# Performance work log

Measured on AMD Instinct MI355X. Metric: run time of the kernel, lower is better.

## Reference

```python
import jax, jax.numpy as jnp
import numpy as np

N_NODES = 50000
N_EDGES = 800000
D_IN, D_HID, D_OUT = 128, 256, 128


def _glorot(key, shape):
    fan_in, fan_out = shape[1], shape[0]
    lim = (6.0 / (fan_in + fan_out)) ** 0.5
    return jax.random.uniform(key, shape, jnp.float32, -lim, lim)


def setup_inputs() -> dict:
    key = jax.random.key(0)
    ks = jax.random.split(key, 8)
    x = jax.random.normal(ks[0], (N_NODES, D_IN), dtype=jnp.float32)
    edge_index = jax.random.randint(ks[1], (2, N_EDGES), 0, N_NODES, dtype=jnp.int64)
    # Layer 1: SAGEConv(D_IN -> D_HID); Layer 2: SAGEConv(D_HID -> D_OUT)
    # PyG SAGEConv: out = lin_l(mean_aggr(x_j)) + lin_r(x); bias lives in lin_l.
    Wl1 = _glorot(ks[2], (D_HID, D_IN))
    bl1 = jnp.zeros((D_HID,), jnp.float32)
    Wr1 = _glorot(ks[3], (D_HID, D_IN))
    Wl2 = _glorot(ks[4], (D_OUT, D_HID))
    bl2 = jnp.zeros((D_OUT,), jnp.float32)
    Wr2 = _glorot(ks[5], (D_OUT, D_HID))
    return {"x": x, "Wl1": Wl1, "bl1": bl1, "Wr1": Wr1,
            "Wl2": Wl2, "bl2": bl2, "Wr2": Wr2, "edge_index": edge_index}


def _sage_conv(x, src, dst, deg_inv, Wl, bl, Wr):
    # gather source features per edge, sum into dst buckets, normalize by in-degree
    msg_sum = jax.ops.segment_sum(x[src], dst, num_segments=N_NODES)  # [N, d_in]
    mean = msg_sum * deg_inv  # mean aggregation; isolated nodes -> zeros
    return mean @ Wl.T + bl + x @ Wr.T


def reference(x, Wl1, bl1, Wr1, Wl2, bl2, Wr2, edge_index):
    src, dst = edge_index[0], edge_index[1]
    deg = jax.ops.segment_sum(jnp.ones((N_EDGES,), jnp.float32), dst,
                              num_segments=N_NODES)
    deg_inv = (1.0 / jnp.maximum(deg, 1.0))[:, None]  # [N, 1]
    h = _sage_conv(x, src, dst, deg_inv, Wl1, bl1, Wr1)
    h = jax.nn.relu(h)  # dropout is identity in eval mode
    out = _sage_conv(h, src, dst, deg_inv, Wl2, bl2, Wr2)
    return out
```

## Files before the change

### kernel.cpp

```cpp
#include <hip/hip_runtime.h>
#include <hip/hip_fp16.h>

#define N_NODES 50000
#define N_EDGES 800000
#define D_IN 128
#define D_HID 256
#define D_OUT 128
#define NCHUNK 196
#define GEMM_GRID 512

typedef _Float16 f16x8 __attribute__((ext_vector_type(8)));
typedef float f32x4 __attribute__((ext_vector_type(4)));


__device__ __forceinline__ void cvt8(const float* __restrict__ src,
                                     __half* __restrict__ dstp, int i) {
    const float4* s4 = (const float4*)src;
    float4 a = s4[i * 2];
    float4 b = s4[i * 2 + 1];
    float4 o;
    __half2* op = (__half2*)&o;
    op[0] = __float22half2_rn(make_float2(a.x, a.y));
    op[1] = __float22half2_rn(make_float2(a.z, a.w));
    op[2] = __float22half2_rn(make_float2(b.x, b.y));
    op[3] = __float22half2_rn(make_float2(b.z, b.w));
    ((float4*)dstp)[i] = o;
}

__global__ __launch_bounds__(256)
void prep_kernel(const float* __restrict__ x, __half* __restrict__ xb,
                 const float* __restrict__ Wl1, const float* __restrict__ Wr1,
                 const float* __restrict__ Wl2, const float* __restrict__ Wr2,
                 __half* __restrict__ wl1h, __half* __restrict__ wr1h,
                 __half* __restrict__ wl2h, __half* __restrict__ wr2h,
                 int* __restrict__ deg) {
    int b = blockIdx.x;
    if (b < 3125) {
        int i = b * 256 + threadIdx.x;
        cvt8(x, xb, i);
    } else if (b < 3141) {
        int i = (b - 3125) * 256 + threadIdx.x;
        cvt8(Wl1, wl1h, i);
        cvt8(Wr1, wr1h, i);
        cvt8(Wl2, wl2h, i);
        cvt8(Wr2, wr2h, i);
    } else {
        int i = (b - 3141) * 256 + threadIdx.x;
        if (i < N_NODES) deg[i] = 0;
    }
}


__global__ void deg_rank_kernel(const int* __restrict__ dst, int* __restrict__ deg,
                                int* __restrict__ rank) {
    int i = blockIdx.x * blockDim.x + threadIdx.x;
    if (i < N_EDGES) rank[i] = atomicAdd(&deg[dst[i]], 1);
}

__global__ void chunk_sum(const int* __restrict__ deg, int* __restrict__ partial) {
    __shared__ int s[256];
    int i = blockIdx.x * 256 + threadIdx.x;
    s[threadIdx.x] = (i < N_NODES) ? deg[i] : 0;
    __syncthreads();
    for (int off = 128; off > 0; off >>= 1) {
        if (threadIdx.x < off) s[threadIdx.x] += s[threadIdx.x + off];
        __syncthreads();
    }
    if (threadIdx.x == 0) partial[blockIdx.x] = s[0];
}

__global__ void scatter_scan(const int* __restrict__ deg, const int* __restrict__ partial,
                             int* __restrict__ row_ptr, float* __restrict__ deg_inv) {
    __shared__ int s[256];
    __shared__ int base_s;
    const int tid = threadIdx.x;
    const int bid = blockIdx.x;
    s[tid] = (tid < bid) ? partial[tid] : 0;
    __syncthreads();
    for (int off = 128; off > 0; off >>= 1) {
        if (tid < off) s[tid] += s[tid + off];
        __syncthreads();
    }
    if (tid == 0) base_s = s[0];
    __syncthreads();
    int i = bid * 256 + tid;
    int v = (i < N_NODES) ? deg[i] : 0;
    s[tid] = v;
    __syncthreads();
    for (int off = 1; off < 256; off <<= 1) {
        int t = (tid >= off) ? s[tid - off] : 0;
        __syncthreads();
        s[tid] += t;
        __syncthreads();
    }
    if (i < N_NODES) {
        int rp = base_s + s[tid] - v;
        row_ptr[i] = rp;
        deg_inv[i] = 1.0f / fmaxf((float)v, 1.0f);
        if (i == N_NODES - 1) row_ptr[N_NODES] = N_EDGES;
    }
}

__global__ void fill_csr(const int* __restrict__ src, const int* __restrict__ dst,
                         const int* __restrict__ rank, const int* __restrict__ row_ptr,
                         int* __restrict__ csr_src) {
    int e = blockIdx.x * blockDim.x + threadIdx.x;
    if (e < N_EDGES) {
        csr_src[row_ptr[dst[e]] + rank[e]] = src[e];
    }
}


__device__ __forceinline__ void add_row(const float4& v, float2 (&acc)[4]) {
    const __half2* hp = (const __half2*)&v;
    #pragma unroll
    for (int j = 0; j < 4; ++j) {
        float2 f = __half22float2(hp[j]);
        acc[j].x += f.x;
        acc[j].y += f.y;
    }
}

template<bool ACCUM_F32>
__device__ __forceinline__ void gather_core(const __half2* __restrict__ feat,
                                            const int* __restrict__ row_ptr,
                                            const int* __restrict__ csr_src,
                                            const float* __restrict__ deg_inv,
                                            __half2* __restrict__ outh,
                                            float* __restrict__ outf) {
    const float4* feat4 = (const float4*)feat;
    const int lane = threadIdx.x & 63;
    const int g = lane >> 4;
    const int s = lane & 15;
    const int n = blockIdx.x * 4 + (threadIdx.x >> 6);
    const int beg = row_ptr[n];
    const int end = row_ptr[n + 1];
    float2 acc[4] = {};

    int idx = (beg + lane < end) ? csr_src[beg + lane] : 0;
    int base = beg;
    while (base < end) {
        int cnt = end - base;
        if (cnt > 64) cnt = 64;
        const int nbase = base + 64;
        int nidx = (nbase + lane < end) ? csr_src[nbase + lane] : 0;

        int it = 0;
        for (; it + 16 <= cnt; it += 16) {
            int s0 = __shfl(idx, it + g);
            int s1 = __shfl(idx, it + 4 + g);
            int s2 = __shfl(idx, it + 8 + g);
            int s3 = __shfl(idx, it + 12 + g);
            float4 v0 = feat4[(size_t)s0 * 16 + s];
            float4 v1 = feat4[(size_t)s1 * 16 + s];
            float4 v2 = feat4[(size_t)s2 * 16 + s];
            float4 v3 = feat4[(size_t)s3 * 16 + s];
            add_row(v0, acc);
            add_row(v1, acc);
            add_row(v2, acc);
            add_row(v3, acc);
        }
        for (; it + 4 <= cnt; it += 4) {
            int s0 = __shfl(idx, it + g);
            float4 v0 = feat4[(size_t)s0 * 16 + s];
            add_row(v0, acc);
        }
        if (it < cnt) {
            int s0 = __shfl(idx, it + g);
            if (g < cnt - it) {
                float4 v0 = feat4[(size_t)s0 * 16 + s];
                add_row(v0, acc);
            }
        }
        idx = nidx;
        base = nbase;
    }

    #pragma unroll
    for (int j = 0; j < 4; ++j) {
        acc[j].x += __shfl_xor(acc[j].x, 16);
        acc[j].y += __shfl_xor(acc[j].y, 16);
        acc[j].x += __shfl_xor(acc[j].x, 32);
        acc[j].y += __shfl_xor(acc[j].y, 32);
    }
    if (g == 0) {
        float di = deg_inv[n];
        if (ACCUM_F32) {
            float4* orow = (float4*)(outf + (size_t)n * 128);
            float4 o0 = orow[s * 2];
            float4 o1 = orow[s * 2 + 1];
            o0.x += acc[0].x * di; o0.y += acc[0].y * di;
            o0.z += acc[1].x * di; o0.w += acc[1].y * di;
            o1.x += acc[2].x * di; o1.y += acc[2].y * di;
            o1.z += acc[3].x * di; o1.w += acc[3].y * di;
            orow[s * 2] = o0;
            orow[s * 2 + 1] = o1;
        } else {
            float4 o;
            __half2* op = (__half2*)&o;
            op[0] = __float22half2_rn(make_float2(acc[0].x * di, acc[0].y * di));
            op[1] = __float22half2_rn(make_float2(acc[1].x * di, acc[1].y * di));
            op[2] = __float22half2_rn(make_float2(acc[2].x * di, acc[2].y * di));
            op[3] = __float22half2_rn(make_float2(acc[3].x * di, acc[3].y * di));
            ((float4*)(outh + (size_t)n * 64))[s] = o;
        }
    }
}

__global__ __launch_bounds__(256)
void gather_mean_h(const __half2* __restrict__ feat, const int* __restrict__ row_ptr,
                   const int* __restrict__ csr_src, const float* __restrict__ deg_inv,
                   __half2* __restrict__ outv) {
    gather_core<false>(feat, row_ptr, csr_src, deg_inv, outv, nullptr);
}

__global__ __launch_bounds__(256)
void gather_mean_add_f32(const __half2* __restrict__ feat, const int* __restrict__ row_ptr,
                         const int* __restrict__ csr_src, const float* __restrict__ deg_inv,
                         float* __restrict__ out) {
    gather_core<true>(feat, row_ptr, csr_src, deg_inv, nullptr, out);
}


#define HPAD 264

__global__ __launch_bounds__(256, 1)
void gemm_fused(const __half* __restrict__ Aa, const __half* __restrict__ Ba,
                const __half* __restrict__ Ab, const __half* __restrict__ Bb,
                const float* __restrict__ bias1,
                const __half* __restrict__ B20, const __half* __restrict__ B21,
                const float* __restrict__ bias2,
                __half* __restrict__ P, float* __restrict__ out) {
    __shared__ __half hlds[2][16][HPAD];
    const int lane = threadIdx.x & 63;
    const int wave = threadIdx.x >> 6;
    const int quad = lane >> 4;
    const int l16 = lane & 15;
    const int koff = quad * 8;

    f16x8 bf1[2][4][4];
    #pragma unroll
    for (int p = 0; p < 2; ++p) {
        const __half* __restrict__ B = p ? Bb : Ba;
        #pragma unroll
        for (int kc = 0; kc < 4; ++kc)
            #pragma unroll
            for (int nt = 0; nt < 4; ++nt)
                bf1[p][kc][nt] = *(const f16x8*)(
                    B + (size_t)(wave * 64 + nt * 16 + l16) * D_IN + kc * 32 + koff);
    }
    float bv1[4];
    #pragma unroll
    for (int nt = 0; nt < 4; ++nt) bv1[nt] = bias1[wave * 64 + nt * 16 + l16];

    f16x8 bf20[8][2], bf21[8][2];
    #pragma unroll
    for (int kc = 0; kc < 8; ++kc)
        #pragma unroll
        for (int nt = 0; nt < 2; ++nt) {
            size_t brow = (size_t)(wave * 32 + nt * 16 + l16) * D_HID + kc * 32 + koff;
            bf20[kc][nt] = *(const f16x8*)(B20 + brow);
            bf21[kc][nt] = *(const f16x8*)(B21 + brow);
        }
    float bv2[2];
    #pragma unroll
    for (int nt = 0; nt < 2; ++nt) bv2[nt] = bias2[wave * 32 + nt * 16 + l16];

    const int NT = N_NODES / 16;
    const int g = gridDim.x;

    auto loadA = [&](int t, f16x8 (&a)[2][4]) {
        const size_t arow = (size_t)(t * 16 + l16) * D_IN + koff;
        #pragma unroll
        for (int kc = 0; kc < 4; ++kc) {
            a[0][kc] = *(const f16x8*)(Aa + arow + kc * 32);
            a[1][kc] = *(const f16x8*)(Ab + arow + kc * 32);
        }
    };

    auto step = [&](int tile, const f16x8 (&a)[2][4], int buf) {
        f32x4 acc1[4] = {};
        #pragma unroll
        for (int p = 0; p < 2; ++p)
            #pragma unroll
            for (int kc = 0; kc < 4; ++kc)
                #pragma unroll
                for (int nt = 0; nt < 4; ++nt)
                    acc1[nt] = __builtin_amdgcn_mfma_f32_16x16x32_f16(
                        a[p][kc], bf1[p][kc][nt], acc1[nt], 0, 0, 0);
        #pragma unroll
        for (int nt = 0; nt < 4; ++nt) {
            int col = wave * 64 + nt * 16 + l16;
            #pragma unroll
            for (int r = 0; r < 4; ++r)
                hlds[buf][quad * 4 + r][col] =
                    __float2half(fmaxf(acc1[nt][r] + bv1[nt], 0.f));
        }
        __syncthreads();
        f32x4 acc20[2] = {};
        f32x4 acc21[2] = {};
        #pragma unroll
        for (int kc = 0; kc < 8; ++kc) {
            f16x8 a2 = *(const f16x8*)&hlds[buf][l16][kc * 32 + koff];
            #pragma unroll
            for (int nt = 0; nt < 2; ++nt) {
                acc20[nt] = __builtin_amdgcn_mfma_f32_16x16x32_f16(
                    a2, bf20[kc][nt], acc20[nt], 0, 0, 0);
                acc21[nt] = __builtin_amdgcn_mfma_f32_16x16x32_f16(
                    a2, bf21[kc][nt], acc21[nt], 0, 0, 0);
            }
        }
        #pragma unroll
        for (int nt = 0; nt < 2; ++nt) {
            int col = wave * 32 + nt * 16 + l16;
            #pragma unroll
            for (int r = 0; r < 4; ++r) {
                int row = tile * 16 + quad * 4 + r;
                P[(size_t)row * D_OUT + col] = __float2half(acc20[nt][r]);
                out[(size_t)row * D_OUT + col] = acc21[nt][r] + bv2[nt];
            }
        }
    };

    f16x8 A0[2][4], A1[2][4];
    int tile = blockIdx.x;
    int buf = 0;
    loadA(tile, A0);
    while (true) {
        if (tile + g < NT) loadA(tile + g, A1);
        step(tile, A0, buf);
        buf ^= 1;
        tile += g;
        if (tile >= NT) break;
        if (tile + g < NT) loadA(tile + g, A0);
        step(tile, A1, buf);
        buf ^= 1;
        tile += g;
        if (tile >= NT) break;
    }
}

extern "C" void kernel_launch(void* const* d_in, const int* in_sizes, int n_in,
                              void* d_out, int out_size, void* d_ws, size_t ws_size,
                              hipStream_t stream) {
    const float* x   = (const float*)d_in[0];
    const float* Wl1 = (const float*)d_in[1];
    const float* bl1 = (const float*)d_in[2];
    const float* Wr1 = (const float*)d_in[3];
    const float* Wl2 = (const float*)d_in[4];
    const float* bl2 = (const float*)d_in[5];
    const float* Wr2 = (const float*)d_in[6];
    const int*   ei  = (const int*)d_in[7];
    const int* src = ei;
    const int* dst = ei + N_EDGES;
    float* out = (float*)d_out;

    char* w = (char*)d_ws;
    auto alloc = [&](size_t bytes) {
        char* r = w;
        w += (bytes + 255) & ~(size_t)255;
        return r;
    };
    int*     deg       = (int*)alloc((size_t)N_NODES * 4);
    int*     row_ptr   = (int*)alloc((size_t)(N_NODES + 1) * 4);
    int*     rank      = (int*)alloc((size_t)N_EDGES * 4);
    int*     partial   = (int*)alloc(NCHUNK * 4);
    int*     csr_src   = (int*)alloc((size_t)N_EDGES * 4);
    float*   deg_inv   = (float*)alloc((size_t)N_NODES * 4);
    __half2* xb        = (__half2*)alloc((size_t)N_NODES * 64 * 4);
    __half2* mean1     = (__half2*)alloc((size_t)N_NODES * 64 * 4);
    __half2* pb        = (__half2*)alloc((size_t)N_NODES * 64 * 4);
    __half*  wl1h      = (__half*)alloc(4 * 32768 * 2);
    __half*  wr1h = wl1h + 32768;
    __half*  wl2h = wr1h + 32768;
    __half*  wr2h = wl2h + 32768;

    prep_kernel<<<3337, 256, 0, stream>>>(x, (__half*)xb, Wl1, Wr1, Wl2, Wr2,
        wl1h, wr1h, wl2h, wr2h, deg);

    deg_rank_kernel<<<(N_EDGES + 255) / 256, 256, 0, stream>>>(dst, deg, rank);
    chunk_sum<<<NCHUNK, 256, 0, stream>>>(deg, partial);
    scatter_scan<<<NCHUNK, 256, 0, stream>>>(deg, partial, row_ptr, deg_inv);
    fill_csr<<<(N_EDGES + 255) / 256, 256, 0, stream>>>(src, dst, rank, row_ptr, csr_src);

    gather_mean_h<<<12500, 256, 0, stream>>>(xb, row_ptr, csr_src, deg_inv, mean1);

    gemm_fused<<<GEMM_GRID, 256, 0, stream>>>(
        (const __half*)mean1, wl1h, (const __half*)xb, wr1h, bl1,
        wl2h, wr2h, bl2, (__half*)pb, out);

    gather_mean_add_f32<<<12500, 256, 0, stream>>>(pb, row_ptr, csr_src, deg_inv, out);
}
```

Baseline: 239.4 us.

## Fuse degree counting into prep, drop chunk-sum, split GEMM into producer/consumer waves

The degree/rank atomic pass is folded into the conversion kernel, with the degree buffer cleared by a memset. The separate chunk-sum kernel is removed: each scan block now re-sums all preceding degrees itself, which adds redundant global reads that grow with block index. The fused GEMM becomes a 512-thread block where four waves compute layer-1 tiles into double-buffered LDS and four other waves consume them for layer 2, so the two stages overlap. The grid is halved to 256 blocks. This cuts kernel launches and aims to overlap the two GEMM stages, at the cost of extra block barriers and a more serial scan.

```diff
diff --git a/kernel.cpp b/kernel.cpp
--- a/kernel.cpp
+++ b/kernel.cpp
@@ -7,7 +7,8 @@
 #define D_HID 256
 #define D_OUT 128
 #define NCHUNK 196
-#define GEMM_GRID 512
+#define NTILES 3125
+#define GEMM_GRID 256
 
 typedef _Float16 f16x8 __attribute__((ext_vector_type(8)));
 typedef float f32x4 __attribute__((ext_vector_type(4)));
@@ -28,12 +29,13 @@
 }
 
 __global__ __launch_bounds__(256)
-void prep_kernel(const float* __restrict__ x, __half* __restrict__ xb,
-                 const float* __restrict__ Wl1, const float* __restrict__ Wr1,
-                 const float* __restrict__ Wl2, const float* __restrict__ Wr2,
-                 __half* __restrict__ wl1h, __half* __restrict__ wr1h,
-                 __half* __restrict__ wl2h, __half* __restrict__ wr2h,
-                 int* __restrict__ deg) {
+void prep_deg_rank(const float* __restrict__ x, __half* __restrict__ xb,
+                   const float* __restrict__ Wl1, const float* __restrict__ Wr1,
+                   const float* __restrict__ Wl2, const float* __restrict__ Wr2,
+                   __half* __restrict__ wl1h, __half* __restrict__ wr1h,
+                   __half* __restrict__ wl2h, __half* __restrict__ wr2h,
+                   const int* __restrict__ dst, int* __restrict__ deg,
+                   int* __restrict__ rank) {
     int b = blockIdx.x;
     if (b < 3125) {
         int i = b * 256 + threadIdx.x;
@@ -45,37 +47,21 @@
         cvt8(Wl2, wl2h, i);
         cvt8(Wr2, wr2h, i);
     } else {
-        int i = (b - 3141) * 256 + threadIdx.x;
-        if (i < N_NODES) deg[i] = 0;
-    }
-}
-
-
-__global__ void deg_rank_kernel(const int* __restrict__ dst, int* __restrict__ deg,
-                                int* __restrict__ rank) {
-    int i = blockIdx.x * blockDim.x + threadIdx.x;
-    if (i < N_EDGES) rank[i] = atomicAdd(&deg[dst[i]], 1);
-}
-
-__global__ void chunk_sum(const int* __restrict__ deg, int* __restrict__ partial) {
-    __shared__ int s[256];
-    int i = blockIdx.x * 256 + threadIdx.x;
-    s[threadIdx.x] = (i < N_NODES) ? deg[i] : 0;
-    __syncthreads();
-    for (int off = 128; off > 0; off >>= 1) {
-        if (threadIdx.x < off) s[threadIdx.x] += s[threadIdx.x + off];
-        __syncthreads();
-    }
-    if (threadIdx.x == 0) partial[blockIdx.x] = s[0];
-}
-
-__global__ void scatter_scan(const int* __restrict__ deg, const int* __restrict__ partial,
+        int e = (b - 3141) * 256 + threadIdx.x;
+        rank[e] = atomicAdd(&deg[dst[e]], 1);
+    }
+}
+
+
+__global__ void scatter_scan(const int* __restrict__ deg,
                              int* __restrict__ row_ptr, float* __restrict__ deg_inv) {
     __shared__ int s[256];
     __shared__ int base_s;
     const int tid = threadIdx.x;
     const int bid = blockIdx.x;
-    s[tid] = (tid < bid) ? partial[tid] : 0;
+    int sum = 0;
+    for (int j = tid; j < bid * 256; j += 256) sum += deg[j];
+    s[tid] = sum;
     __syncthreads();
     for (int off = 128; off > 0; off >>= 1) {
         if (tid < off) s[tid] += s[tid + off];
@@ -224,119 +210,134 @@
 
 #define HPAD 264
 
-__global__ __launch_bounds__(256, 1)
-void gemm_fused(const __half* __restrict__ Aa, const __half* __restrict__ Ba,
-                const __half* __restrict__ Ab, const __half* __restrict__ Bb,
-                const float* __restrict__ bias1,
-                const __half* __restrict__ B20, const __half* __restrict__ B21,
-                const float* __restrict__ bias2,
-                __half* __restrict__ P, float* __restrict__ out) {
-    __shared__ __half hlds[2][16][HPAD];
+__global__ __launch_bounds__(512, 1)
+void gemm_pc(const __half* __restrict__ Aa,
+             const __half* __restrict__ Ab,
+             const __half* __restrict__ Wl1h, const __half* __restrict__ Wr1h,
+             const float* __restrict__ bias1,
+             const __half* __restrict__ B20, const __half* __restrict__ B21,
+             const float* __restrict__ bias2,
+             __half* __restrict__ P, float* __restrict__ out) {
+    __shared__ __half ldsH[2][16][HPAD];
     const int lane = threadIdx.x & 63;
     const int wave = threadIdx.x >> 6;
     const int quad = lane >> 4;
     const int l16 = lane & 15;
     const int koff = quad * 8;
-
-    f16x8 bf1[2][4][4];
-    #pragma unroll
-    for (int p = 0; p < 2; ++p) {
-        const __half* __restrict__ B = p ? Bb : Ba;
+    const int g = gridDim.x;
+
+    if (wave < 4) {
+        f16x8 bf1[2][4][4];
         #pragma unroll
-        for (int kc = 0; kc < 4; ++kc)
-            #pragma unroll
-            for (int nt = 0; nt < 4; ++nt)
-                bf1[p][kc][nt] = *(const f16x8*)(
-                    B + (size_t)(wave * 64 + nt * 16 + l16) * D_IN + kc * 32 + koff);
-    }
-    float bv1[4];
-    #pragma unroll
-    for (int nt = 0; nt < 4; ++nt) bv1[nt] = bias1[wave * 64 + nt * 16 + l16];
-
-    f16x8 bf20[8][2], bf21[8][2];
-    #pragma unroll
-    for (int kc = 0; kc < 8; ++kc)
+        for (int p = 0; p < 2; ++p) {
+            const __half* __restrict__ B = p ? Wr1h : Wl1h;
+            #pragma unroll
+            for (int kc = 0; kc < 4; ++kc)
+                #pragma unroll
+                for (int nt = 0; nt < 4; ++nt)
+                    bf1[p][kc][nt] = *(const f16x8*)(
+                        B + (size_t)(wave * 64 + nt * 16 + l16) * D_IN + kc * 32 + koff);
+        }
+        float bv1[4];
         #pragma unroll
-        for (int nt = 0; nt < 2; ++nt) {
-            size_t brow = (size_t)(wave * 32 + nt * 16 + l16) * D_HID + kc * 32 + koff;
-            bf20[kc][nt] = *(const f16x8*)(B20 + brow);
-            bf21[kc][nt] = *(const f16x8*)(B21 + brow);
-        }
-    float bv2[2];
-    #pragma unroll
-    for (int nt = 0; nt < 2; ++nt) bv2[nt] = bias2[wave * 32 + nt * 16 + l16];
-
-    const int NT = N_NODES / 16;
-    const int g = gridDim.x;
-
-    auto loadA = [&](int t, f16x8 (&a)[2][4]) {
-        const size_t arow = (size_t)(t * 16 + l16) * D_IN + koff;
+        for (int nt = 0; nt < 4; ++nt) bv1[nt] = bias1[wave * 64 + nt * 16 + l16];
+
+        auto loadA = [&](int t, f16x8 (&am)[4], f16x8 (&ax)[4]) {
+            const size_t arow = (size_t)(t * 16 + l16) * D_IN + koff;
+            #pragma unroll
+            for (int kc = 0; kc < 4; ++kc) {
+                am[kc] = *(const f16x8*)(Aa + arow + kc * 32);
+                ax[kc] = *(const f16x8*)(Ab + arow + kc * 32);
+            }
+        };
+        auto produce = [&](const f16x8 (&am)[4], const f16x8 (&ax)[4], int buf) {
+            f32x4 acc1[4] = {};
+            #pragma unroll
+            for (int kc = 0; kc < 4; ++kc)
+                #pragma unroll
+                for (int nt = 0; nt < 4; ++nt) {
+                    acc1[nt] = __builtin_amdgcn_mfma_f32_16x16x32_f16(
+                        am[kc], bf1[0][kc][nt], acc1[nt], 0, 0, 0);
+                    acc1[nt] = __builtin_amdgcn_mfma_f32_16x16x32_f16(
+                        ax[kc], bf1[1][kc][nt], acc1[nt], 0, 0, 0);
+                }
+            #pragma unroll
+            for (int nt = 0; nt < 4; ++nt) {
+                int col = wave * 64 + nt * 16 + l16;
+                #pragma unroll
+                for (int r = 0; r < 4; ++r)
+                    ldsH[buf][quad * 4 + r][col] =
+                        __float2half(fmaxf(acc1[nt][r] + bv1[nt], 0.f));
+            }
+        };
+
+        f16x8 am0[4], ax0[4], am1[4], ax1[4];
+        int tile = blockIdx.x;
+        loadA(tile, am0, ax0);
+        while (true) {
+            if (tile + g < NTILES) loadA(tile + g, am1, ax1);
+            produce(am0, ax0, 0);
+            __syncthreads();
+            tile += g;
+            if (tile >= NTILES) break;
+            if (tile + g < NTILES) loadA(tile + g, am0, ax0);
+            produce(am1, ax1, 1);
+            __syncthreads();
+            tile += g;
+            if (tile >= NTILES) break;
+        }
+    } else {
+        const int cw = wave - 4;
+        f16x8 bf20[8][2], bf21[8][2];
         #pragma unroll
-        for (int kc = 0; kc < 4; ++kc) {
-            a[0][kc] = *(const f16x8*)(Aa + arow + kc * 32);
-            a[1][kc] = *(const f16x8*)(Ab + arow + kc * 32);
-        }
-    };
-
-    auto step = [&](int tile, const f16x8 (&a)[2][4], int buf) {
-        f32x4 acc1[4] = {};
+        for (int kc = 0; kc < 8; ++kc)
+            #pragma unroll
+            for (int nt = 0; nt < 2; ++nt) {
+                size_t brow = (size_t)(cw * 32 + nt * 16 + l16) * D_HID + kc * 32 + koff;
+                bf20[kc][nt] = *(const f16x8*)(B20 + brow);
+                bf21[kc][nt] = *(const f16x8*)(B21 + brow);
+            }
+        float bv2[2];
         #pragma unroll
-        for (int p = 0; p < 2; ++p)
-            #pragma unroll
-            for (int kc = 0; kc < 4; ++kc)
-                #pragma unroll
-                for (int nt = 0; nt < 4; ++nt)
-                    acc1[nt] = __builtin_amdgcn_mfma_f32_16x16x32_f16(
-                        a[p][kc], bf1[p][kc][nt], acc1[nt], 0, 0, 0);
-        #pragma unroll
-        for (int nt = 0; nt < 4; ++nt) {
-            int col = wave * 64 + nt * 16 + l16;
-            #pragma unroll
-            for (int r = 0; r < 4; ++r)
-                hlds[buf][quad * 4 + r][col] =
-                    __float2half(fmaxf(acc1[nt][r] + bv1[nt], 0.f));
-        }
-        __syncthreads();
-        f32x4 acc20[2] = {};
-        f32x4 acc21[2] = {};
-        #pragma unroll
-        for (int kc = 0; kc < 8; ++kc) {
-            f16x8 a2 = *(const f16x8*)&hlds[buf][l16][kc * 32 + koff];
+        for (int nt = 0; nt < 2; ++nt) bv2[nt] = bias2[cw * 32 + nt * 16 + l16];
+
+        auto consume = [&](int t, int buf) {
+            f32x4 acc20[2] = {};
+            f32x4 acc21[2] = {};
+            #pragma unroll
+            for (int kc = 0; kc < 8; ++kc) {
+                f16x8 a2 = *(const f16x8*)&ldsH[buf][l16][kc * 32 + koff];
+                #pragma unroll
+                for (int nt = 0; nt < 2; ++nt) {
+                    acc20[nt] = __builtin_amdgcn_mfma_f32_16x16x32_f16(
+                        a2, bf20[kc][nt], acc20[nt], 0, 0, 0);
+                    acc21[nt] = __builtin_amdgcn_mfma_f32_16x16x32_f16(
+                        a2, bf21[kc][nt], acc21[nt], 0, 0, 0);
+                }
+            }
             #pragma unroll
             for (int nt = 0; nt < 2; ++nt) {
-                acc20[nt] = __builtin_amdgcn_mfma_f32_16x16x32_f16(
-                    a2, bf20[kc][nt], acc20[nt], 0, 0, 0);
-                acc21[nt] = __builtin_amdgcn_mfma_f32_16x16x32_f16(
-                    a2, bf21[kc][nt], acc21[nt], 0, 0, 0);
-            }
-        }
-        #pragma unroll
-        for (int nt = 0; nt < 2; ++nt) {
-            int col = wave * 32 + nt * 16 + l16;
-            #pragma unroll
-            for (int r = 0; r < 4; ++r) {
-                int row = tile * 16 + quad * 4 + r;
-                P[(size_t)row * D_OUT + col] = __float2half(acc20[nt][r]);
-                out[(size_t)row * D_OUT + col] = acc21[nt][r] + bv2[nt];
-            }
-        }
-    };
-
-    f16x8 A0[2][4], A1[2][4];
-    int tile = blockIdx.x;
-    int buf = 0;
-    loadA(tile, A0);
-    while (true) {
-        if (tile + g < NT) loadA(tile + g, A1);
-        step(tile, A0, buf);
-        buf ^= 1;
-        tile += g;
-        if (tile >= NT) break;
-        if (tile + g < NT) loadA(tile + g, A0);
-        step(tile, A1, buf);
-        buf ^= 1;
-        tile += g;
-        if (tile >= NT) break;
+                int col = cw * 32 + nt * 16 + l16;
+                #pragma unroll
+                for (int r = 0; r < 4; ++r) {
+                    int row = t * 16 + quad * 4 + r;
+                    P[(size_t)row * D_OUT + col] = __float2half(acc20[nt][r]);
+                    out[(size_t)row * D_OUT + col] = acc21[nt][r] + bv2[nt];
+                }
+            }
+        };
+
+        int tile = blockIdx.x;
+        int prevTile = -1, prevBuf = 0, buf = 0;
+        while (tile < NTILES) {
+            if (prevTile >= 0) consume(prevTile, prevBuf);
+            __syncthreads();
+            prevTile = tile;
+            prevBuf = buf;
+            buf ^= 1;
+            tile += g;
+        }
+        if (prevTile >= 0) consume(prevTile, prevBuf);
     }
 }
 
@@ -364,7 +365,6 @@
     int*     deg       = (int*)alloc((size_t)N_NODES * 4);
     int*     row_ptr   = (int*)alloc((size_t)(N_NODES + 1) * 4);
     int*     rank      = (int*)alloc((size_t)N_EDGES * 4);
-    int*     partial   = (int*)alloc(NCHUNK * 4);
     int*     csr_src   = (int*)alloc((size_t)N_EDGES * 4);
     float*   deg_inv   = (float*)alloc((size_t)N_NODES * 4);
     __half2* xb        = (__half2*)alloc((size_t)N_NODES * 64 * 4);
@@ -375,18 +375,18 @@
     __half*  wl2h = wr1h + 32768;
     __half*  wr2h = wl2h + 32768;
 
-    prep_kernel<<<3337, 256, 0, stream>>>(x, (__half*)xb, Wl1, Wr1, Wl2, Wr2,
-        wl1h, wr1h, wl2h, wr2h, deg);
-
-    deg_rank_kernel<<<(N_EDGES + 255) / 256, 256, 0, stream>>>(dst, deg, rank);
-    chunk_sum<<<NCHUNK, 256, 0, stream>>>(deg, partial);
-    scatter_scan<<<NCHUNK, 256, 0, stream>>>(deg, partial, row_ptr, deg_inv);
+    hipMemsetAsync(deg, 0, (size_t)N_NODES * 4, stream);
+
+    prep_deg_rank<<<6266, 256, 0, stream>>>(x, (__half*)xb, Wl1, Wr1, Wl2, Wr2,
+        wl1h, wr1h, wl2h, wr2h, dst, deg, rank);
+
+    scatter_scan<<<NCHUNK, 256, 0, stream>>>(deg, row_ptr, deg_inv);
     fill_csr<<<(N_EDGES + 255) / 256, 256, 0, stream>>>(src, dst, rank, row_ptr, csr_src);
 
     gather_mean_h<<<12500, 256, 0, stream>>>(xb, row_ptr, csr_src, deg_inv, mean1);
 
-    gemm_fused<<<GEMM_GRID, 256, 0, stream>>>(
-        (const __half*)mean1, wl1h, (const __half*)xb, wr1h, bl1,
+    gemm_pc<<<GEMM_GRID, 512, 0, stream>>>(
+        (const __half*)mean1, (const __half*)xb, wl1h, wr1h, bl1,
         wl2h, wr2h, bl2, (__half*)pb, out);
 
     gather_mean_add_f32<<<12500, 256, 0, stream>>>(pb, row_ptr, csr_src, deg_inv, out);
```

Result: slower. 253.1 us (+5.7%).
